# Performance work log

Measured on AMD Instinct MI355X. Metric: run time of the kernel, lower is better.

Reference implementation:

```python
import jax, jax.numpy as jnp
import numpy as np

N = 4_194_304

def setup_inputs() -> dict:
    key = jax.random.key(0)
    k1, k2 = jax.random.split(key)
    preds = jax.random.normal(k1, (N, 5), dtype=jnp.float32)
    target = jax.random.normal(k2, (N, 3), dtype=jnp.float32)
    return {"preds": preds, "target": target}

def reference(preds, target):
    # main MSE on first 3 columns: [N, 3]
    main_mse = (preds[:, :3] - target[:, :3]) ** 2

    p2 = preds[:, 2]
    p3 = preds[:, 3]
    p4 = preds[:, 4]
    t2 = target[:, 2]

    # lower-range loss (note: original multiplies by 2**2 == 4, not squares, in first branch)
    lower = jnp.where(
        p3 > p2,
        (p4 - t2) * 4.0,
        jnp.where(p3 > t2 * 0.95, 0.0, (p3 - t2 * 0.95) ** 2),
    )
    # upper-range loss
    upper = jnp.where(
        p4 < p2,
        (p4 - t2) * 4.0,
        jnp.where(p4 < t2 * 1.05, 0.0, (p4 - t2 * 1.05) ** 2),
    )

    loss = jnp.concatenate([main_mse, lower[:, None], upper[:, None]], axis=1)  # [N, 5]
    return jnp.mean(loss)
```

## Files before the change

kernel.cpp:

```cpp
#include <hip/hip_runtime.h>


#define BLOCK 256
#define ROWS_PER_THREAD 4

__device__ __forceinline__ float row_loss(float p0, float p1, float p2,
                                          float p3, float p4,
                                          float t0, float t1, float t2) {
    float d0 = p0 - t0, d1 = p1 - t1, d2 = p2 - t2;
    float acc = d0 * d0 + d1 * d1 + d2 * d2;
    float tl = t2 * 0.95f;
    float tu = t2 * 1.05f;
    float pen = (p4 - t2) * 4.0f;
    float dl = p3 - tl;
    float du = p4 - tu;
    float lower = (p3 > p2) ? pen : ((p3 > tl) ? 0.0f : dl * dl);
    float upper = (p4 < p2) ? pen : ((p4 < tu) ? 0.0f : du * du);
    return acc + lower + upper;
}

__global__ __launch_bounds__(BLOCK) void ql_main(const float* __restrict__ preds,
                                                 const float* __restrict__ target,
                                                 double* __restrict__ ws,
                                                 int rows) {
    long tid = (long)blockIdx.x * BLOCK + threadIdx.x;
    long r0 = tid * ROWS_PER_THREAD;
    float acc = 0.0f;

    if (r0 + ROWS_PER_THREAD - 1 < rows) {
        const float4* pp = (const float4*)(preds + r0 * 5);
        const float4* tp = (const float4*)(target + r0 * 3);
        union { float4 v[5]; float f[20]; } P;
        union { float4 v[3]; float f[12]; } T;
        P.v[0] = pp[0]; P.v[1] = pp[1]; P.v[2] = pp[2]; P.v[3] = pp[3]; P.v[4] = pp[4];
        T.v[0] = tp[0]; T.v[1] = tp[1]; T.v[2] = tp[2];
#pragma unroll
        for (int j = 0; j < ROWS_PER_THREAD; ++j) {
            acc += row_loss(P.f[5 * j + 0], P.f[5 * j + 1], P.f[5 * j + 2],
                            P.f[5 * j + 3], P.f[5 * j + 4],
                            T.f[3 * j + 0], T.f[3 * j + 1], T.f[3 * j + 2]);
        }
    } else {
        for (long r = r0; r < rows && r < r0 + ROWS_PER_THREAD; ++r) {
            const float* p = preds + r * 5;
            const float* t = target + r * 3;
            acc += row_loss(p[0], p[1], p[2], p[3], p[4], t[0], t[1], t[2]);
        }
    }

    double dacc = (double)acc;
#pragma unroll
    for (int off = 32; off > 0; off >>= 1)
        dacc += __shfl_down(dacc, off, 64);

    __shared__ double wsum[BLOCK / 64];
    int lane = threadIdx.x & 63;
    int wave = threadIdx.x >> 6;
    if (lane == 0) wsum[wave] = dacc;
    __syncthreads();

    if (threadIdx.x == 0) {
        double b = 0.0;
#pragma unroll
        for (int w = 0; w < BLOCK / 64; ++w) b += wsum[w];
        atomicAdd(ws, b);
    }
}

__global__ void ql_finalize(const double* __restrict__ ws, float* __restrict__ out, long rows) {
    out[0] = (float)(ws[0] / (double)(rows * 5));
}

extern "C" void kernel_launch(void* const* d_in, const int* in_sizes, int n_in,
                              void* d_out, int out_size, void* d_ws, size_t ws_size,
                              hipStream_t stream) {
    const float* preds = (const float*)d_in[0];
    const float* target = (const float*)d_in[1];
    long rows = (long)in_sizes[0] / 5;

    double* acc = (double*)d_ws;
    hipMemsetAsync(acc, 0, sizeof(double), stream);

    long threads_needed = (rows + ROWS_PER_THREAD - 1) / ROWS_PER_THREAD;
    int blocks = (int)((threads_needed + BLOCK - 1) / BLOCK);

    ql_main<<<blocks, BLOCK, 0, stream>>>(preds, target, acc, (int)rows);
    ql_finalize<<<1, 1, 0, stream>>>(acc, (float*)d_out, rows);
}
```

Baseline: 176.5 us.

## Stage row tiles through shared memory with coalesced float4 loads, one row per thread

Each block now cooperatively loads a 256-row tile of preds and target into shared memory using contiguous float4 loads, so each wave's global accesses are fully coalesced. Each thread then reads one row from LDS and computes its loss. This replaces the per-thread strided 4-row float4 loads, whose access pattern spanned several cache lines per wave instruction. In exchange it quadruples the block count and therefore the number of atomics and reductions, adds an LDS round trip and a barrier, and the strided LDS reads may bank-conflict.

```diff
diff --git a/kernel.cpp b/kernel.cpp
--- a/kernel.cpp
+++ b/kernel.cpp
@@ -2,7 +2,7 @@
 
 
 #define BLOCK 256
-#define ROWS_PER_THREAD 4
+#define TILE  256
 
 __device__ __forceinline__ float row_loss(float p0, float p1, float p2,
                                           float p3, float p4,
@@ -22,47 +22,56 @@
 __global__ __launch_bounds__(BLOCK) void ql_main(const float* __restrict__ preds,
                                                  const float* __restrict__ target,
                                                  double* __restrict__ ws,
-                                                 int rows) {
-    long tid = (long)blockIdx.x * BLOCK + threadIdx.x;
-    long r0 = tid * ROWS_PER_THREAD;
-    float acc = 0.0f;
+                                                 long rows) {
+    __shared__ float sp[TILE * 5];
+    __shared__ float st[TILE * 3];
+    __shared__ double wsum[BLOCK / 64];
 
-    if (r0 + ROWS_PER_THREAD - 1 < rows) {
-        const float4* pp = (const float4*)(preds + r0 * 5);
-        const float4* tp = (const float4*)(target + r0 * 3);
-        union { float4 v[5]; float f[20]; } P;
-        union { float4 v[3]; float f[12]; } T;
-        P.v[0] = pp[0]; P.v[1] = pp[1]; P.v[2] = pp[2]; P.v[3] = pp[3]; P.v[4] = pp[4];
-        T.v[0] = tp[0]; T.v[1] = tp[1]; T.v[2] = tp[2];
-#pragma unroll
-        for (int j = 0; j < ROWS_PER_THREAD; ++j) {
-            acc += row_loss(P.f[5 * j + 0], P.f[5 * j + 1], P.f[5 * j + 2],
-                            P.f[5 * j + 3], P.f[5 * j + 4],
-                            T.f[3 * j + 0], T.f[3 * j + 1], T.f[3 * j + 2]);
+    const int t = threadIdx.x;
+    const long row0 = (long)blockIdx.x * TILE;
+    float loss = 0.0f;
+
+    if (row0 + TILE <= rows) {
+        const float4* pbase = (const float4*)(preds + row0 * 5);
+        const float4* tbase = (const float4*)(target + row0 * 3);
+        float4* sp4 = (float4*)sp;
+        float4* st4 = (float4*)st;
+
+        sp4[t] = pbase[t];
+        int k2 = t + 256;
+        if (k2 < TILE * 5 / 4) {
+            sp4[k2] = pbase[k2];
+        } else {
+            int m = k2 - TILE * 5 / 4;
+            st4[m] = tbase[m];
         }
+        __syncthreads();
+
+        loss = row_loss(sp[5 * t + 0], sp[5 * t + 1], sp[5 * t + 2],
+                        sp[5 * t + 3], sp[5 * t + 4],
+                        st[3 * t + 0], st[3 * t + 1], st[3 * t + 2]);
     } else {
-        for (long r = r0; r < rows && r < r0 + ROWS_PER_THREAD; ++r) {
+        long r = row0 + t;
+        if (r < rows) {
             const float* p = preds + r * 5;
-            const float* t = target + r * 3;
-            acc += row_loss(p[0], p[1], p[2], p[3], p[4], t[0], t[1], t[2]);
+            const float* tg = target + r * 3;
+            loss = row_loss(p[0], p[1], p[2], p[3], p[4], tg[0], tg[1], tg[2]);
         }
+        __syncthreads();
     }
 
-    double dacc = (double)acc;
+    double dacc = (double)loss;
 #pragma unroll
     for (int off = 32; off > 0; off >>= 1)
         dacc += __shfl_down(dacc, off, 64);
 
-    __shared__ double wsum[BLOCK / 64];
-    int lane = threadIdx.x & 63;
-    int wave = threadIdx.x >> 6;
+    int lane = t & 63;
+    int wave = t >> 6;
     if (lane == 0) wsum[wave] = dacc;
     __syncthreads();
 
-    if (threadIdx.x == 0) {
-        double b = 0.0;
-#pragma unroll
-        for (int w = 0; w < BLOCK / 64; ++w) b += wsum[w];
+    if (t == 0) {
+        double b = wsum[0] + wsum[1] + wsum[2] + wsum[3];
         atomicAdd(ws, b);
     }
 }
@@ -81,9 +90,7 @@
     double* acc = (double*)d_ws;
     hipMemsetAsync(acc, 0, sizeof(double), stream);
 
-    long threads_needed = (rows + ROWS_PER_THREAD - 1) / ROWS_PER_THREAD;
-    int blocks = (int)((threads_needed + BLOCK - 1) / BLOCK);
-
-    ql_main<<<blocks, BLOCK, 0, stream>>>(preds, target, acc, (int)rows);
+    int blocks = (int)((rows + TILE - 1) / TILE);
+    ql_main<<<blocks, BLOCK, 0, stream>>>(preds, target, acc, rows);
     ql_finalize<<<1, 1, 0, stream>>>(acc, (float*)d_out, rows);
 }
```

Result: slower. 318.9 us (+80.7%).

## Use persistent wave-tiled grid with LDS staging and per-block partials

Applied to the files above, without the earlier changes.

Each wave now loads a 64-row tile using fully coalesced float4 loads. It stages the tile through LDS so each lane can read its own row, and it prefetches the next tile in registers. The grid is fixed at 1024 blocks that loop over tiles. Each block writes its partial sum to its own slot instead of doing a global atomic, which removes the memset. The finalize kernel sums the partials and handles the tail rows. The aim is better coalescing and less atomic and launch overhead, at the cost of LDS traffic, possible bank conflicts from the stride-5 reads, and fewer resident blocks.

```diff
diff --git a/kernel.cpp b/kernel.cpp
--- a/kernel.cpp
+++ b/kernel.cpp
@@ -2,7 +2,8 @@
 
 
 #define BLOCK 256
-#define ROWS_PER_THREAD 4
+#define NBLK  1024
+#define WAVES_PER_BLOCK (BLOCK / 64)
 
 __device__ __forceinline__ float row_loss(float p0, float p1, float p2,
                                           float p3, float p4,
@@ -22,53 +23,88 @@
 __global__ __launch_bounds__(BLOCK) void ql_main(const float* __restrict__ preds,
                                                  const float* __restrict__ target,
                                                  double* __restrict__ ws,
-                                                 int rows) {
-    long tid = (long)blockIdx.x * BLOCK + threadIdx.x;
-    long r0 = tid * ROWS_PER_THREAD;
+                                                 long ntiles) {
+    __shared__ float4 sbuf[WAVES_PER_BLOCK][128];
+    __shared__ double wsum[WAVES_PER_BLOCK];
+
+    const int lane = threadIdx.x & 63;
+    const int w = threadIdx.x >> 6;
+    const long gwave = (long)blockIdx.x * WAVES_PER_BLOCK + w;
+    const long nw = (long)gridDim.x * WAVES_PER_BLOCK;
+
+    const float4* pb4 = (const float4*)preds;
+    const float4* tb4 = (const float4*)target;
+    float* sp = (float*)&sbuf[w][0];
+    float* st = (float*)&sbuf[w][80];
+
     float acc = 0.0f;
+    long t = gwave;
+    bool have = t < ntiles;
+    float4 r0, r1;
+    if (have) {
+        r0 = pb4[t * 80 + lane];
+        r1 = (lane < 16) ? pb4[t * 80 + 64 + lane] : tb4[t * 48 + (lane - 16)];
+    }
 
-    if (r0 + ROWS_PER_THREAD - 1 < rows) {
-        const float4* pp = (const float4*)(preds + r0 * 5);
-        const float4* tp = (const float4*)(target + r0 * 3);
-        union { float4 v[5]; float f[20]; } P;
-        union { float4 v[3]; float f[12]; } T;
-        P.v[0] = pp[0]; P.v[1] = pp[1]; P.v[2] = pp[2]; P.v[3] = pp[3]; P.v[4] = pp[4];
-        T.v[0] = tp[0]; T.v[1] = tp[1]; T.v[2] = tp[2];
-#pragma unroll
-        for (int j = 0; j < ROWS_PER_THREAD; ++j) {
-            acc += row_loss(P.f[5 * j + 0], P.f[5 * j + 1], P.f[5 * j + 2],
-                            P.f[5 * j + 3], P.f[5 * j + 4],
-                            T.f[3 * j + 0], T.f[3 * j + 1], T.f[3 * j + 2]);
+    while (have) {
+        sbuf[w][lane] = r0;
+        sbuf[w][(lane < 16) ? (64 + lane) : (80 + lane - 16)] = r1;
+
+        long tn = t + nw;
+        bool haven = tn < ntiles;
+        if (haven) {
+            r0 = pb4[tn * 80 + lane];
+            r1 = (lane < 16) ? pb4[tn * 80 + 64 + lane] : tb4[tn * 48 + (lane - 16)];
         }
-    } else {
-        for (long r = r0; r < rows && r < r0 + ROWS_PER_THREAD; ++r) {
-            const float* p = preds + r * 5;
-            const float* t = target + r * 3;
-            acc += row_loss(p[0], p[1], p[2], p[3], p[4], t[0], t[1], t[2]);
-        }
+
+        acc += row_loss(sp[5 * lane + 0], sp[5 * lane + 1], sp[5 * lane + 2],
+                        sp[5 * lane + 3], sp[5 * lane + 4],
+                        st[3 * lane + 0], st[3 * lane + 1], st[3 * lane + 2]);
+
+        t = tn;
+        have = haven;
     }
 
     double dacc = (double)acc;
 #pragma unroll
     for (int off = 32; off > 0; off >>= 1)
         dacc += __shfl_down(dacc, off, 64);
-
-    __shared__ double wsum[BLOCK / 64];
-    int lane = threadIdx.x & 63;
-    int wave = threadIdx.x >> 6;
-    if (lane == 0) wsum[wave] = dacc;
+    if (lane == 0) wsum[w] = dacc;
     __syncthreads();
-
-    if (threadIdx.x == 0) {
-        double b = 0.0;
-#pragma unroll
-        for (int w = 0; w < BLOCK / 64; ++w) b += wsum[w];
-        atomicAdd(ws, b);
-    }
+    if (threadIdx.x == 0)
+        ws[blockIdx.x] = wsum[0] + wsum[1] + wsum[2] + wsum[3];
 }
 
-__global__ void ql_finalize(const double* __restrict__ ws, float* __restrict__ out, long rows) {
-    out[0] = (float)(ws[0] / (double)(rows * 5));
+__global__ __launch_bounds__(256) void ql_finalize(const double* __restrict__ ws,
+                                                   const float* __restrict__ preds,
+                                                   const float* __restrict__ target,
+                                                   float* __restrict__ out,
+                                                   long rows, long tail_start) {
+    __shared__ double wsum[4];
+    const int tid = threadIdx.x;
+
+    double d = 0.0;
+#pragma unroll
+    for (int i = 0; i < NBLK / 256; ++i)
+        d += ws[tid + i * 256];
+
+    long r = tail_start + tid;
+    if (r < rows) {
+        const float* p = preds + r * 5;
+        const float* tg = target + r * 3;
+        d += (double)row_loss(p[0], p[1], p[2], p[3], p[4], tg[0], tg[1], tg[2]);
+    }
+
+#pragma unroll
+    for (int off = 32; off > 0; off >>= 1)
+        d += __shfl_down(d, off, 64);
+    int lane = tid & 63, w = tid >> 6;
+    if (lane == 0) wsum[w] = d;
+    __syncthreads();
+    if (tid == 0) {
+        double total = wsum[0] + wsum[1] + wsum[2] + wsum[3];
+        out[0] = (float)(total / ((double)rows * 5.0));
+    }
 }
 
 extern "C" void kernel_launch(void* const* d_in, const int* in_sizes, int n_in,
@@ -77,13 +113,12 @@
     const float* preds = (const float*)d_in[0];
     const float* target = (const float*)d_in[1];
     long rows = (long)in_sizes[0] / 5;
+    long ntiles = rows / 64;
+    long tail_start = ntiles * 64;
 
-    double* acc = (double*)d_ws;
-    hipMemsetAsync(acc, 0, sizeof(double), stream);
+    double* partials = (double*)d_ws;
 
-    long threads_needed = (rows + ROWS_PER_THREAD - 1) / ROWS_PER_THREAD;
-    int blocks = (int)((threads_needed + BLOCK - 1) / BLOCK);
-
-    ql_main<<<blocks, BLOCK, 0, stream>>>(preds, target, acc, (int)rows);
-    ql_finalize<<<1, 1, 0, stream>>>(acc, (float*)d_out, rows);
+    ql_main<<<NBLK, BLOCK, 0, stream>>>(preds, target, partials, ntiles);
+    ql_finalize<<<1, 256, 0, stream>>>(partials, preds, target,
+                                       (float*)d_out, rows, tail_start);
 }
```

After: 157.4 us. -10.9%, faster.
